# Optimization experiments

Hardware: AMD Instinct MI355X
Metric: run time of the kernel (lower is better)

## Reference

```python
import jax, jax.numpy as jnp
import numpy as np

N0, N1, N2, N3 = 400000, 100000, 20000, 4096
IN_F, HID_F, OUT_F = 256, 256, 128
E0, E1, E2 = 1500000, 200000, 40960


def setup_inputs() -> dict:
    key = jax.random.key(0)
    ks = jax.random.split(key, 16)
    inp = {}
    inp['feat'] = jax.random.normal(ks[0], (N0, IN_F), dtype=jnp.float32)
    inp['e0_src'] = jax.random.randint(ks[1], (E0,), 0, N0)
    inp['e0_dst'] = jax.random.randint(ks[2], (E0,), 0, N1)
    inp['e1_src'] = jax.random.randint(ks[3], (E1,), 0, N1)
    inp['e1_dst'] = jax.random.randint(ks[4], (E1,), 0, N2)
    inp['e2_src'] = jax.random.randint(ks[5], (E2,), 0, N2)
    inp['e2_dst'] = jax.random.randint(ks[6], (E2,), 0, N3)
    # SAGEConv params: fc_self and fc_neigh weights (in,out) + shared bias
    def lin(k, fi, fo):
        s = 1.0 / np.sqrt(fi)
        return jax.random.uniform(k, (fi, fo), jnp.float32, -s, s)
    inp['w_self0'] = lin(ks[7], IN_F, HID_F)
    inp['w_neigh0'] = lin(ks[8], IN_F, HID_F)
    inp['b0'] = jnp.zeros((HID_F,), jnp.float32)
    inp['w_self1'] = lin(ks[9], HID_F, HID_F)
    inp['w_neigh1'] = lin(ks[10], HID_F, HID_F)
    inp['b1'] = jnp.zeros((HID_F,), jnp.float32)
    inp['w_self2'] = lin(ks[11], HID_F, OUT_F)
    inp['w_neigh2'] = lin(ks[12], HID_F, OUT_F)
    inp['b2'] = jnp.zeros((OUT_F,), jnp.float32)
    return inp


def _sage_conv(h, src, dst, n_dst, w_self, w_neigh, b, act):
    # mean aggregation of src-node features onto dst nodes (irregular gather + segment reduce)
    msgs = h[src]                                                  # [E, F]
    s = jax.ops.segment_sum(msgs, dst, num_segments=n_dst)        # [n_dst, F]
    cnt = jax.ops.segment_sum(jnp.ones((src.shape[0], 1), h.dtype), dst, num_segments=n_dst)
    h_neigh = s / jnp.maximum(cnt, 1.0)
    out = h[:n_dst] @ w_self + h_neigh @ w_neigh + b
    return jax.nn.relu(out) if act else out


def reference(feat, e0_src, e0_dst, e1_src, e1_dst, e2_src, e2_dst,
              w_self0, w_neigh0, b0, w_self1, w_neigh1, b1, w_self2, w_neigh2, b2):
    # dropout is identity (eval mode)
    h = _sage_conv(feat, e0_src, e0_dst, N1, w_self0, w_neigh0, b0, act=True)
    h = _sage_conv(h, e1_src, e1_dst, N2, w_self1, w_neigh1, b1, act=True)
    h = _sage_conv(h, e2_src, e2_dst, N3, w_self2, w_neigh2, b2, act=False)
    return h
```

## Files before the change

### kernel.cpp

```cpp
#include <hip/hip_runtime.h>
#include <hip/hip_bf16.h>


static constexpr int kN1 = 100000, kN2 = 20000, kN3 = 4096;
static constexpr int kE0 = 1500000, kE1 = 200000, kE2 = 40960;

using bf8v  = __attribute__((ext_vector_type(8))) short;
using f32x4 = __attribute__((ext_vector_type(4))) float;

__device__ __forceinline__ unsigned short f2bu(float f) {
    __hip_bfloat16 h = __float2bfloat16(f);
    return *reinterpret_cast<unsigned short*>(&h);
}
__device__ __forceinline__ float bu2f_lo(unsigned u) {
    unsigned b = u << 16; return *reinterpret_cast<float*>(&b);
}
__device__ __forceinline__ float bu2f_hi(unsigned u) {
    unsigned b = u & 0xffff0000u; return *reinterpret_cast<float*>(&b);
}

static constexpr int CB  = 50000;
static constexpr int C0B = (kE0 + 255) / 256;
static constexpr int C1B = (kE1 + 255) / 256;
static constexpr int C2B = (kE2 + 255) / 256;
static constexpr int PW0B = 512, PW1B = 512, PW2B = 256;
static constexpr int M4_0 = kN1 / 4, M4_1 = kN2 / 4, M4_2 = kN3 / 4;
static constexpr int B0 = (M4_0 + 255) / 256;
static constexpr int B1 = (M4_1 + 255) / 256;
static constexpr int B2 = (M4_2 + 255) / 256;
static constexpr int ZN4 = (kN1 + kN2 + kN3) / 4;
static constexpr int ZB  = (ZN4 + 255) / 256;

__global__ __launch_bounds__(256) void k_zero(int4* __restrict__ p)
{
    int i = blockIdx.x * 256 + threadIdx.x;
    if (i < ZN4) p[i] = make_int4(0, 0, 0, 0);
}

template <bool BIG>
__global__ __launch_bounds__(256) void k_phase0(
    const float4* __restrict__ feat4, uint4* __restrict__ featbf,
    const int* __restrict__ e0d, const int* __restrict__ e1d,
    const int* __restrict__ e2d,
    int* __restrict__ cnt0, int* __restrict__ cnt1, int* __restrict__ cnt2,
    const float* __restrict__ ws0, const float* __restrict__ wn0,
    const float* __restrict__ ws1, const float* __restrict__ wn1,
    const float* __restrict__ ws2, const float* __restrict__ wn2,
    unsigned short* __restrict__ wt0, unsigned short* __restrict__ wt1,
    unsigned short* __restrict__ wt2)
{
    int b = blockIdx.x;
    const int tid = threadIdx.x;
    if (BIG) {
        if (b < CB) {
            int i = b * 256 + tid;
            float4 a = feat4[2 * i], c = feat4[2 * i + 1];
            uint4 o;
            o.x = (unsigned)f2bu(a.x) | ((unsigned)f2bu(a.y) << 16);
            o.y = (unsigned)f2bu(a.z) | ((unsigned)f2bu(a.w) << 16);
            o.z = (unsigned)f2bu(c.x) | ((unsigned)f2bu(c.y) << 16);
            o.w = (unsigned)f2bu(c.z) | ((unsigned)f2bu(c.w) << 16);
            featbf[i] = o;
            return;
        }
        b -= CB;
    }
    if (b < C0B) {
        int e = b * 256 + tid;
        if (e < kE0) atomicAdd(cnt0 + e0d[e], 1);
        return;
    }
    b -= C0B;
    if (b < C1B) {
        int e = b * 256 + tid;
        if (e < kE1) atomicAdd(cnt1 + e1d[e], 1);
        return;
    }
    b -= C1B;
    if (b < C2B) {
        int e = b * 256 + tid;
        if (e < kE2) atomicAdd(cnt2 + e2d[e], 1);
        return;
    }
    b -= C2B;
    if (b < PW0B) {
        int idx = b * 256 + tid;
        int n = idx >> 9, k = idx & 511;
        wt0[idx] = f2bu(k < 256 ? ws0[k * 256 + n] : wn0[(k - 256) * 256 + n]);
        return;
    }
    b -= PW0B;
    if (b < PW1B) {
        int idx = b * 256 + tid;
        int n = idx >> 9, k = idx & 511;
        wt1[idx] = f2bu(k < 256 ? ws1[k * 256 + n] : wn1[(k - 256) * 256 + n]);
        return;
    }
    b -= PW1B;
    {
        int idx = b * 256 + tid;
        int n = idx >> 9, k = idx & 511;
        wt2[idx] = f2bu(k < 256 ? ws2[k * 128 + n] : wn2[(k - 256) * 128 + n]);
    }
}

__global__ __launch_bounds__(256) void k_bsum_all(
    const int* __restrict__ cnt0, const int* __restrict__ cnt1,
    const int* __restrict__ cnt2, int* __restrict__ bsum)
{
    const int* cnt; int lb, M4, bo;
    int b = blockIdx.x;
    if (b < B0)            { cnt = cnt0; lb = b;            M4 = M4_0; bo = 0; }
    else if (b < B0 + B1)  { cnt = cnt1; lb = b - B0;       M4 = M4_1; bo = B0; }
    else                   { cnt = cnt2; lb = b - B0 - B1;  M4 = M4_2; bo = B0 + B1; }
    __shared__ int wsum[4];
    int idx = lb * 256 + threadIdx.x;
    int ts = 0;
    if (idx < M4) {
        int4 v = reinterpret_cast<const int4*>(cnt)[idx];
        ts = v.x + v.y + v.z + v.w;
    }
#pragma unroll
    for (int off = 32; off > 0; off >>= 1) ts += __shfl_down(ts, off, 64);
    if ((threadIdx.x & 63) == 0) wsum[threadIdx.x >> 6] = ts;
    __syncthreads();
    if (threadIdx.x == 0)
        bsum[bo + lb] = wsum[0] + wsum[1] + wsum[2] + wsum[3];
}

__global__ __launch_bounds__(256) void k_bscan_all(int* __restrict__ bsum)
{
    __shared__ int s[B0 + B1 + B2];
    const int total = B0 + B1 + B2;
    if (threadIdx.x < total) s[threadIdx.x] = bsum[threadIdx.x];
    __syncthreads();
    if (threadIdx.x < 3) {
        int lo = threadIdx.x == 0 ? 0 : (threadIdx.x == 1 ? B0 : B0 + B1);
        int hi = threadIdx.x == 0 ? B0 : (threadIdx.x == 1 ? B0 + B1 : total);
        int run = 0;
        for (int i = lo; i < hi; ++i) { int v = s[i]; s[i] = run; run += v; }
    }
    __syncthreads();
    if (threadIdx.x < total) bsum[threadIdx.x] = s[threadIdx.x];
}

__global__ __launch_bounds__(256) void k_bapply_all(
    const int* __restrict__ cnt0, const int* __restrict__ cnt1,
    const int* __restrict__ cnt2, const int* __restrict__ bsum,
    int* __restrict__ rp0, int* __restrict__ rp1, int* __restrict__ rp2)
{
    const int* cnt; int* rp; int lb, M4, bo;
    int b = blockIdx.x;
    if (b < B0)            { cnt = cnt0; rp = rp0; lb = b;           M4 = M4_0; bo = 0; }
    else if (b < B0 + B1)  { cnt = cnt1; rp = rp1; lb = b - B0;      M4 = M4_1; bo = B0; }
    else                   { cnt = cnt2; rp = rp2; lb = b - B0 - B1; M4 = M4_2; bo = B0 + B1; }
    __shared__ int wsum[4];
    __shared__ int wexcl[4];
    const int lane = threadIdx.x & 63;
    const int wid = threadIdx.x >> 6;
    int idx = lb * 256 + threadIdx.x;
    int4 v = make_int4(0, 0, 0, 0);
    if (idx < M4) v = reinterpret_cast<const int4*>(cnt)[idx];
    int ts = v.x + v.y + v.z + v.w;
    int incl = ts;
#pragma unroll
    for (int off = 1; off < 64; off <<= 1) {
        int t = __shfl_up(incl, off, 64);
        if (lane >= off) incl += t;
    }
    if (lane == 63) wsum[wid] = incl;
    __syncthreads();
    if (threadIdx.x < 4) {
        int e = 0;
        for (int i = 0; i < (int)threadIdx.x; ++i) e += wsum[i];
        wexcl[threadIdx.x] = e;
    }
    __syncthreads();
    if (idx < M4) {
        int base = bsum[bo + lb] + wexcl[wid] + (incl - ts);
        int4 o;
        o.x = base;
        o.y = base + v.x;
        o.z = base + v.x + v.y;
        o.w = base + v.x + v.y + v.z;
        reinterpret_cast<int4*>(rp)[idx] = o;
    }
}

__global__ __launch_bounds__(256) void k_fill_all(
    const int* __restrict__ e0s, const int* __restrict__ e0d,
    const int* __restrict__ e1s, const int* __restrict__ e1d,
    const int* __restrict__ e2s, const int* __restrict__ e2d,
    int* __restrict__ rp0, int* __restrict__ rp1, int* __restrict__ rp2,
    int* __restrict__ csr0, int* __restrict__ csr1, int* __restrict__ csr2)
{
    int b = blockIdx.x;
    const int* src; const int* dst; int* rp; int* csr; int E, lb;
    if (b < C0B)            { src = e0s; dst = e0d; rp = rp0; csr = csr0; E = kE0; lb = b; }
    else if (b < C0B + C1B) { src = e1s; dst = e1d; rp = rp1; csr = csr1; E = kE1; lb = b - C0B; }
    else                    { src = e2s; dst = e2d; rp = rp2; csr = csr2; E = kE2; lb = b - C0B - C1B; }
    int e = lb * 256 + threadIdx.x;
    if (e < E) {
        int pos = atomicAdd(rp + dst[e], 1);
        csr[pos] = src[e];
    }
}

__global__ __launch_bounds__(256) void k_gather_agg_b(
    const unsigned short* __restrict__ h, const int* __restrict__ csr,
    const int* __restrict__ rp_end, const int* __restrict__ cnt,
    unsigned short* __restrict__ agg, int M)
{
    int d = blockIdx.x * 4 + (threadIdx.x >> 6);
    if (d >= M) return;
    const int lane = threadIdx.x & 63;
    const int half = lane >> 5;
    const int l32 = lane & 31;
    int c = cnt[d], end = rp_end[d], start = end - c;
    float a[8] = {0.f, 0.f, 0.f, 0.f, 0.f, 0.f, 0.f, 0.f};
    for (int chunk = start; chunk < end; chunk += 64) {
        int n = end - chunk; if (n > 64) n = 64;
        int mysrc = (lane < n) ? csr[chunk + lane] : 0;
#pragma unroll 4
        for (int e = 0; e < n; e += 2) {
            int ie = e + half;
            int s = __shfl(mysrc, ie, 64);
            if (ie < n) {
                uint4 v = *reinterpret_cast<const uint4*>(
                    h + (size_t)s * 256 + l32 * 8);
                a[0] += bu2f_lo(v.x); a[1] += bu2f_hi(v.x);
                a[2] += bu2f_lo(v.y); a[3] += bu2f_hi(v.y);
                a[4] += bu2f_lo(v.z); a[5] += bu2f_hi(v.z);
                a[6] += bu2f_lo(v.w); a[7] += bu2f_hi(v.w);
            }
        }
    }
#pragma unroll
    for (int j = 0; j < 8; ++j) a[j] += __shfl(a[j], lane ^ 32, 64);
    if (half == 0) {
        float inv = 1.0f / (float)(c > 1 ? c : 1);
        uint4 o;
        o.x = (unsigned)f2bu(a[0] * inv) | ((unsigned)f2bu(a[1] * inv) << 16);
        o.y = (unsigned)f2bu(a[2] * inv) | ((unsigned)f2bu(a[3] * inv) << 16);
        o.z = (unsigned)f2bu(a[4] * inv) | ((unsigned)f2bu(a[5] * inv) << 16);
        o.w = (unsigned)f2bu(a[6] * inv) | ((unsigned)f2bu(a[7] * inv) << 16);
        *reinterpret_cast<uint4*>(agg + (size_t)d * 256 + l32 * 8) = o;
    }
}

__global__ __launch_bounds__(256) void k_gather_agg_f(
    const float* __restrict__ h, const int* __restrict__ csr,
    const int* __restrict__ rp_end, const int* __restrict__ cnt,
    unsigned short* __restrict__ agg, int M)
{
    int d = blockIdx.x * 4 + (threadIdx.x >> 6);
    if (d >= M) return;
    int lane = threadIdx.x & 63;
    int c = cnt[d], end = rp_end[d], start = end - c;
    float a0 = 0.f, a1 = 0.f, a2 = 0.f, a3 = 0.f;
    for (int chunk = start; chunk < end; chunk += 64) {
        int n = end - chunk; if (n > 64) n = 64;
        int mysrc = (lane < n) ? csr[chunk + lane] : 0;
#pragma unroll 4
        for (int e = 0; e < n; ++e) {
            int s = __shfl(mysrc, e, 64);
            float4 v = reinterpret_cast<const float4*>(h + (size_t)s * 256)[lane];
            a0 += v.x; a1 += v.y; a2 += v.z; a3 += v.w;
        }
    }
    float inv = 1.0f / (float)(c > 1 ? c : 1);
    ushort4 o;
    o.x = f2bu(a0 * inv); o.y = f2bu(a1 * inv);
    o.z = f2bu(a2 * inv); o.w = f2bu(a3 * inv);
    *reinterpret_cast<ushort4*>(agg + (size_t)d * 256 + lane * 4) = o;
}

template <int ACT, bool A0F32, bool OUTF32>
__global__ __launch_bounds__(256) void k_mfma_gemm(
    const void* __restrict__ A0v, const unsigned short* __restrict__ A1,
    const unsigned short* __restrict__ WT, const float* __restrict__ bias,
    void* __restrict__ outv, int M, int N)
{
    __shared__ unsigned short sA[128 * 72];
    __shared__ unsigned short sB[128 * 72];
    const int tid = threadIdx.x;
    const int lane = tid & 63;
    const int w = tid >> 6;
    const int wr = w >> 1, wc = w & 1;
    const int row0 = blockIdx.x * 128;
    const int col0 = blockIdx.y * 128;

    f32x4 acc[4][4] = {};

    for (int p = 0; p < 8; ++p) {
        const int kc0 = p * 64;
        if (kc0 < 256) {
            if constexpr (A0F32) {
                const float* src = (const float*)A0v;
#pragma unroll
                for (int ps = 0; ps < 8; ++ps) {
                    int flat = (ps * 256 + tid) * 4;
                    int r = flat >> 6, cc = flat & 63;
                    int row = row0 + r; row = row < M ? row : M - 1;
                    float4 v = *reinterpret_cast<const float4*>(
                        src + (size_t)row * 256 + kc0 + cc);
                    ushort4 b4;
                    b4.x = f2bu(v.x); b4.y = f2bu(v.y);
                    b4.z = f2bu(v.z); b4.w = f2bu(v.w);
                    *reinterpret_cast<ushort4*>(&sA[r * 72 + cc]) = b4;
                }
            } else {
                const unsigned short* src = (const unsigned short*)A0v;
#pragma unroll
                for (int ps = 0; ps < 4; ++ps) {
                    int f8 = ps * 256 + tid;
                    int r = f8 >> 3, c8 = f8 & 7;
                    int row = row0 + r; row = row < M ? row : M - 1;
                    uint4 v = *reinterpret_cast<const uint4*>(
                        src + (size_t)row * 256 + kc0 + c8 * 8);
                    *reinterpret_cast<uint4*>(&sA[r * 72 + c8 * 8]) = v;
                }
            }
        } else {
#pragma unroll
            for (int ps = 0; ps < 4; ++ps) {
                int f8 = ps * 256 + tid;
                int r = f8 >> 3, c8 = f8 & 7;
                int row = row0 + r; row = row < M ? row : M - 1;
                uint4 v = *reinterpret_cast<const uint4*>(
                    A1 + (size_t)row * 256 + (kc0 - 256) + c8 * 8);
                *reinterpret_cast<uint4*>(&sA[r * 72 + c8 * 8]) = v;
            }
        }
#pragma unroll
        for (int ps = 0; ps < 4; ++ps) {
            int f8 = ps * 256 + tid;
            int r = f8 >> 3, c8 = f8 & 7;
            uint4 v = *reinterpret_cast<const uint4*>(
                WT + (size_t)(col0 + r) * 512 + kc0 + c8 * 8);
            *reinterpret_cast<uint4*>(&sB[r * 72 + c8 * 8]) = v;
        }
        __syncthreads();
#pragma unroll
        for (int ks = 0; ks < 64; ks += 32) {
            const int lr = lane & 15;
            const int kk = ks + (lane >> 4) * 8;
            bf8v af[4], bfr[4];
#pragma unroll
            for (int m = 0; m < 4; ++m)
                af[m] = *reinterpret_cast<const bf8v*>(
                    &sA[(wr * 64 + m * 16 + lr) * 72 + kk]);
#pragma unroll
            for (int n = 0; n < 4; ++n)
                bfr[n] = *reinterpret_cast<const bf8v*>(
                    &sB[(wc * 64 + n * 16 + lr) * 72 + kk]);
#pragma unroll
            for (int m = 0; m < 4; ++m)
#pragma unroll
                for (int n = 0; n < 4; ++n)
                    acc[m][n] = __builtin_amdgcn_mfma_f32_16x16x32_bf16(
                        af[m], bfr[n], acc[m][n], 0, 0, 0);
        }
        __syncthreads();
    }

    const int lc = lane & 15;
    const int lr4 = (lane >> 4) * 4;
#pragma unroll
    for (int n = 0; n < 4; ++n) {
        int col = col0 + wc * 64 + n * 16 + lc;
        float bb = bias[col];
#pragma unroll
        for (int m = 0; m < 4; ++m) {
#pragma unroll
            for (int j = 0; j < 4; ++j) {
                int row = row0 + wr * 64 + m * 16 + lr4 + j;
                if (row < M) {
                    float v = acc[m][n][j] + bb;
                    if (ACT) v = fmaxf(v, 0.f);
                    if constexpr (OUTF32)
                        ((float*)outv)[(size_t)row * N + col] = v;
                    else
                        ((unsigned short*)outv)[(size_t)row * N + col] = f2bu(v);
                }
            }
        }
    }
}

extern "C" void kernel_launch(void* const* d_in, const int* in_sizes, int n_in,
                              void* d_out, int out_size, void* d_ws, size_t ws_size,
                              hipStream_t stream) {
    const float* feat = (const float*)d_in[0];
    const int* e0s = (const int*)d_in[1];
    const int* e0d = (const int*)d_in[2];
    const int* e1s = (const int*)d_in[3];
    const int* e1d = (const int*)d_in[4];
    const int* e2s = (const int*)d_in[5];
    const int* e2d = (const int*)d_in[6];
    const float* ws0 = (const float*)d_in[7];
    const float* wn0 = (const float*)d_in[8];
    const float* b0 = (const float*)d_in[9];
    const float* ws1 = (const float*)d_in[10];
    const float* wn1 = (const float*)d_in[11];
    const float* b1 = (const float*)d_in[12];
    const float* ws2 = (const float*)d_in[13];
    const float* wn2 = (const float*)d_in[14];
    const float* b2 = (const float*)d_in[15];
    float* out = (float*)d_out;

    char* base = (char*)d_ws;
    const bool big = ws_size >= 330000000ull;
    unsigned short* featbf = nullptr;
    size_t off = 0;
    if (big) { featbf = (unsigned short*)base; off += 204800000ull; }
    unsigned short* aggb = (unsigned short*)(base + off); off += 51200000ull;
    unsigned short* h1b  = (unsigned short*)(base + off); off += 51200000ull;
    unsigned short* h2b  = (unsigned short*)(base + off); off += 10240000ull;
    unsigned short* wt0  = (unsigned short*)(base + off); off += 262144ull;
    unsigned short* wt1  = (unsigned short*)(base + off); off += 262144ull;
    unsigned short* wt2  = (unsigned short*)(base + off); off += 131072ull;
    int* csr0 = (int*)(base + off); off += 6000000ull;
    int* csr1 = (int*)(base + off); off += 800000ull;
    int* csr2 = (int*)(base + off); off += 163840ull;
    int* cnt0 = (int*)(base + off); off += 400000ull;
    int* cnt1 = (int*)(base + off); off += 80000ull;
    int* cnt2 = (int*)(base + off); off += 16384ull;
    int* rp0  = (int*)(base + off); off += 400000ull;
    int* rp1  = (int*)(base + off); off += 80000ull;
    int* rp2  = (int*)(base + off); off += 16384ull;
    int* bsum = (int*)(base + off); off += 512ull;

    k_zero<<<ZB, 256, 0, stream>>>((int4*)cnt0);

    if (big)
        k_phase0<true><<<CB + C0B + C1B + C2B + PW0B + PW1B + PW2B, 256, 0, stream>>>(
            (const float4*)feat, (uint4*)featbf, e0d, e1d, e2d,
            cnt0, cnt1, cnt2, ws0, wn0, ws1, wn1, ws2, wn2, wt0, wt1, wt2);
    else
        k_phase0<false><<<C0B + C1B + C2B + PW0B + PW1B + PW2B, 256, 0, stream>>>(
            nullptr, nullptr, e0d, e1d, e2d,
            cnt0, cnt1, cnt2, ws0, wn0, ws1, wn1, ws2, wn2, wt0, wt1, wt2);

    k_bsum_all<<<B0 + B1 + B2, 256, 0, stream>>>(cnt0, cnt1, cnt2, bsum);
    k_bscan_all<<<1, 256, 0, stream>>>(bsum);
    k_bapply_all<<<B0 + B1 + B2, 256, 0, stream>>>(
        cnt0, cnt1, cnt2, bsum, rp0, rp1, rp2);
    k_fill_all<<<C0B + C1B + C2B, 256, 0, stream>>>(
        e0s, e0d, e1s, e1d, e2s, e2d, rp0, rp1, rp2, csr0, csr1, csr2);

    if (big) {
        k_gather_agg_b<<<(kN1 + 3) / 4, 256, 0, stream>>>(
            featbf, csr0, rp0, cnt0, aggb, kN1);
        k_mfma_gemm<1, false, false><<<dim3(782, 2), 256, 0, stream>>>(
            featbf, aggb, wt0, b0, h1b, kN1, 256);
    } else {
        k_gather_agg_f<<<(kN1 + 3) / 4, 256, 0, stream>>>(
            feat, csr0, rp0, cnt0, aggb, kN1);
        k_mfma_gemm<1, true, false><<<dim3(782, 2), 256, 0, stream>>>(
            feat, aggb, wt0, b0, h1b, kN1, 256);
    }

    k_gather_agg_b<<<(kN2 + 3) / 4, 256, 0, stream>>>(
        h1b, csr1, rp1, cnt1, aggb, kN2);
    k_mfma_gemm<1, false, false><<<dim3(157, 2), 256, 0, stream>>>(
        h1b, aggb, wt1, b1, h2b, kN2, 256);

    k_gather_agg_b<<<(kN3 + 3) / 4, 256, 0, stream>>>(
        h2b, csr2, rp2, cnt2, aggb, kN3);
    k_mfma_gemm<0, false, true><<<dim3(32, 1), 256, 0, stream>>>(
        h2b, aggb, wt2, b2, out, kN3, 128);
}
```

Before: 565.1 us.

## Fuse CSR-build front-end kernels into one persistent kernel with grid barriers

Replaces the phase0, block-sum, block-scan, scan-apply and fill kernels with a single persistent kernel of 1024 blocks. The blocks loop over virtual block indices and separate the phases with atomic-counter grid barriers. The zeroed region is widened so the barrier counters are cleared each call. This removes four kernel launches and their gaps. The costs are fewer resident blocks for the large streaming conversion phase and spin-wait barriers, which deadlock if all 1024 blocks are not co-resident.

```diff
diff --git a/kernel.cpp b/kernel.cpp
--- a/kernel.cpp
+++ b/kernel.cpp
@@ -28,8 +28,10 @@
 static constexpr int B0 = (M4_0 + 255) / 256;
 static constexpr int B1 = (M4_1 + 255) / 256;
 static constexpr int B2 = (M4_2 + 255) / 256;
-static constexpr int ZN4 = (kN1 + kN2 + kN3) / 4;
+static constexpr int BSCAN = B0 + B1 + B2;
+static constexpr int ZN4 = 496448 / 16;
 static constexpr int ZB  = (ZN4 + 255) / 256;
+static constexpr int NB = 1024;
 
 __global__ __launch_bounds__(256) void k_zero(int4* __restrict__ p)
 {
@@ -37,172 +39,174 @@
     if (i < ZN4) p[i] = make_int4(0, 0, 0, 0);
 }
 
+__device__ __forceinline__ void gbar(int* ctr)
+{
+    __syncthreads();
+    if (threadIdx.x == 0) {
+        __threadfence();
+        atomicAdd(ctr, 1);
+        while (atomicAdd(ctr, 0) < NB) __builtin_amdgcn_s_sleep(8);
+        __threadfence();
+    }
+    __syncthreads();
+}
+
 template <bool BIG>
-__global__ __launch_bounds__(256) void k_phase0(
+__global__ __launch_bounds__(256, 4) void k_megafront(
     const float4* __restrict__ feat4, uint4* __restrict__ featbf,
-    const int* __restrict__ e0d, const int* __restrict__ e1d,
-    const int* __restrict__ e2d,
+    const int* __restrict__ e0s, const int* __restrict__ e0d,
+    const int* __restrict__ e1s, const int* __restrict__ e1d,
+    const int* __restrict__ e2s, const int* __restrict__ e2d,
     int* __restrict__ cnt0, int* __restrict__ cnt1, int* __restrict__ cnt2,
     const float* __restrict__ ws0, const float* __restrict__ wn0,
     const float* __restrict__ ws1, const float* __restrict__ wn1,
     const float* __restrict__ ws2, const float* __restrict__ wn2,
     unsigned short* __restrict__ wt0, unsigned short* __restrict__ wt1,
-    unsigned short* __restrict__ wt2)
-{
-    int b = blockIdx.x;
+    unsigned short* __restrict__ wt2,
+    int* __restrict__ bsum,
+    int* __restrict__ rp0, int* __restrict__ rp1, int* __restrict__ rp2,
+    int* __restrict__ csr0, int* __restrict__ csr1, int* __restrict__ csr2,
+    int* __restrict__ gctr)
+{
+    __shared__ int smem[128];
+    __shared__ int sreg[128];
     const int tid = threadIdx.x;
-    if (BIG) {
-        if (b < CB) {
-            int i = b * 256 + tid;
-            float4 a = feat4[2 * i], c = feat4[2 * i + 1];
-            uint4 o;
-            o.x = (unsigned)f2bu(a.x) | ((unsigned)f2bu(a.y) << 16);
-            o.y = (unsigned)f2bu(a.z) | ((unsigned)f2bu(a.w) << 16);
-            o.z = (unsigned)f2bu(c.x) | ((unsigned)f2bu(c.y) << 16);
-            o.w = (unsigned)f2bu(c.z) | ((unsigned)f2bu(c.w) << 16);
-            featbf[i] = o;
-            return;
-        }
-        b -= CB;
-    }
-    if (b < C0B) {
-        int e = b * 256 + tid;
-        if (e < kE0) atomicAdd(cnt0 + e0d[e], 1);
-        return;
-    }
-    b -= C0B;
-    if (b < C1B) {
-        int e = b * 256 + tid;
-        if (e < kE1) atomicAdd(cnt1 + e1d[e], 1);
-        return;
-    }
-    b -= C1B;
-    if (b < C2B) {
-        int e = b * 256 + tid;
-        if (e < kE2) atomicAdd(cnt2 + e2d[e], 1);
-        return;
-    }
-    b -= C2B;
-    if (b < PW0B) {
-        int idx = b * 256 + tid;
-        int n = idx >> 9, k = idx & 511;
-        wt0[idx] = f2bu(k < 256 ? ws0[k * 256 + n] : wn0[(k - 256) * 256 + n]);
-        return;
-    }
-    b -= PW0B;
-    if (b < PW1B) {
-        int idx = b * 256 + tid;
-        int n = idx >> 9, k = idx & 511;
-        wt1[idx] = f2bu(k < 256 ? ws1[k * 256 + n] : wn1[(k - 256) * 256 + n]);
-        return;
-    }
-    b -= PW1B;
-    {
-        int idx = b * 256 + tid;
-        int n = idx >> 9, k = idx & 511;
-        wt2[idx] = f2bu(k < 256 ? ws2[k * 128 + n] : wn2[(k - 256) * 128 + n]);
-    }
-}
-
-__global__ __launch_bounds__(256) void k_bsum_all(
-    const int* __restrict__ cnt0, const int* __restrict__ cnt1,
-    const int* __restrict__ cnt2, int* __restrict__ bsum)
-{
-    const int* cnt; int lb, M4, bo;
-    int b = blockIdx.x;
-    if (b < B0)            { cnt = cnt0; lb = b;            M4 = M4_0; bo = 0; }
-    else if (b < B0 + B1)  { cnt = cnt1; lb = b - B0;       M4 = M4_1; bo = B0; }
-    else                   { cnt = cnt2; lb = b - B0 - B1;  M4 = M4_2; bo = B0 + B1; }
-    __shared__ int wsum[4];
-    int idx = lb * 256 + threadIdx.x;
-    int ts = 0;
-    if (idx < M4) {
-        int4 v = reinterpret_cast<const int4*>(cnt)[idx];
-        ts = v.x + v.y + v.z + v.w;
-    }
-#pragma unroll
-    for (int off = 32; off > 0; off >>= 1) ts += __shfl_down(ts, off, 64);
-    if ((threadIdx.x & 63) == 0) wsum[threadIdx.x >> 6] = ts;
-    __syncthreads();
-    if (threadIdx.x == 0)
-        bsum[bo + lb] = wsum[0] + wsum[1] + wsum[2] + wsum[3];
-}
-
-__global__ __launch_bounds__(256) void k_bscan_all(int* __restrict__ bsum)
-{
-    __shared__ int s[B0 + B1 + B2];
-    const int total = B0 + B1 + B2;
-    if (threadIdx.x < total) s[threadIdx.x] = bsum[threadIdx.x];
-    __syncthreads();
-    if (threadIdx.x < 3) {
-        int lo = threadIdx.x == 0 ? 0 : (threadIdx.x == 1 ? B0 : B0 + B1);
-        int hi = threadIdx.x == 0 ? B0 : (threadIdx.x == 1 ? B0 + B1 : total);
-        int run = 0;
-        for (int i = lo; i < hi; ++i) { int v = s[i]; s[i] = run; run += v; }
-    }
-    __syncthreads();
-    if (threadIdx.x < total) bsum[threadIdx.x] = s[threadIdx.x];
-}
-
-__global__ __launch_bounds__(256) void k_bapply_all(
-    const int* __restrict__ cnt0, const int* __restrict__ cnt1,
-    const int* __restrict__ cnt2, const int* __restrict__ bsum,
-    int* __restrict__ rp0, int* __restrict__ rp1, int* __restrict__ rp2)
-{
-    const int* cnt; int* rp; int lb, M4, bo;
-    int b = blockIdx.x;
-    if (b < B0)            { cnt = cnt0; rp = rp0; lb = b;           M4 = M4_0; bo = 0; }
-    else if (b < B0 + B1)  { cnt = cnt1; rp = rp1; lb = b - B0;      M4 = M4_1; bo = B0; }
-    else                   { cnt = cnt2; rp = rp2; lb = b - B0 - B1; M4 = M4_2; bo = B0 + B1; }
-    __shared__ int wsum[4];
-    __shared__ int wexcl[4];
-    const int lane = threadIdx.x & 63;
-    const int wid = threadIdx.x >> 6;
-    int idx = lb * 256 + threadIdx.x;
-    int4 v = make_int4(0, 0, 0, 0);
-    if (idx < M4) v = reinterpret_cast<const int4*>(cnt)[idx];
-    int ts = v.x + v.y + v.z + v.w;
-    int incl = ts;
-#pragma unroll
-    for (int off = 1; off < 64; off <<= 1) {
-        int t = __shfl_up(incl, off, 64);
-        if (lane >= off) incl += t;
-    }
-    if (lane == 63) wsum[wid] = incl;
-    __syncthreads();
-    if (threadIdx.x < 4) {
-        int e = 0;
-        for (int i = 0; i < (int)threadIdx.x; ++i) e += wsum[i];
-        wexcl[threadIdx.x] = e;
-    }
-    __syncthreads();
-    if (idx < M4) {
-        int base = bsum[bo + lb] + wexcl[wid] + (incl - ts);
-        int4 o;
-        o.x = base;
-        o.y = base + v.x;
-        o.z = base + v.x + v.y;
-        o.w = base + v.x + v.y + v.z;
-        reinterpret_cast<int4*>(rp)[idx] = o;
-    }
-}
-
-__global__ __launch_bounds__(256) void k_fill_all(
-    const int* __restrict__ e0s, const int* __restrict__ e0d,
-    const int* __restrict__ e1s, const int* __restrict__ e1d,
-    const int* __restrict__ e2s, const int* __restrict__ e2d,
-    int* __restrict__ rp0, int* __restrict__ rp1, int* __restrict__ rp2,
-    int* __restrict__ csr0, int* __restrict__ csr1, int* __restrict__ csr2)
-{
-    int b = blockIdx.x;
-    const int* src; const int* dst; int* rp; int* csr; int E, lb;
-    if (b < C0B)            { src = e0s; dst = e0d; rp = rp0; csr = csr0; E = kE0; lb = b; }
-    else if (b < C0B + C1B) { src = e1s; dst = e1d; rp = rp1; csr = csr1; E = kE1; lb = b - C0B; }
-    else                    { src = e2s; dst = e2d; rp = rp2; csr = csr2; E = kE2; lb = b - C0B - C1B; }
-    int e = lb * 256 + threadIdx.x;
-    if (e < E) {
-        int pos = atomicAdd(rp + dst[e], 1);
-        csr[pos] = src[e];
+
+    const int P0 = (BIG ? CB : 0) + C0B + C1B + C2B + PW0B + PW1B + PW2B;
+    for (int vb = blockIdx.x; vb < P0; vb += NB) {
+        int b = vb;
+        bool done = false;
+        if (BIG) {
+            if (b < CB) {
+                int i = b * 256 + tid;
+                float4 a = feat4[2 * i], c = feat4[2 * i + 1];
+                uint4 o;
+                o.x = (unsigned)f2bu(a.x) | ((unsigned)f2bu(a.y) << 16);
+                o.y = (unsigned)f2bu(a.z) | ((unsigned)f2bu(a.w) << 16);
+                o.z = (unsigned)f2bu(c.x) | ((unsigned)f2bu(c.y) << 16);
+                o.w = (unsigned)f2bu(c.z) | ((unsigned)f2bu(c.w) << 16);
+                featbf[i] = o;
+                done = true;
+            } else b -= CB;
+        }
+        if (!done && b < C0B) {
+            int e = b * 256 + tid;
+            if (e < kE0) atomicAdd(cnt0 + e0d[e], 1);
+            done = true;
+        } else if (!done) b -= C0B;
+        if (!done && b < C1B) {
+            int e = b * 256 + tid;
+            if (e < kE1) atomicAdd(cnt1 + e1d[e], 1);
+            done = true;
+        } else if (!done) b -= C1B;
+        if (!done && b < C2B) {
+            int e = b * 256 + tid;
+            if (e < kE2) atomicAdd(cnt2 + e2d[e], 1);
+            done = true;
+        } else if (!done) b -= C2B;
+        if (!done && b < PW0B) {
+            int idx = b * 256 + tid;
+            int n = idx >> 9, k = idx & 511;
+            wt0[idx] = f2bu(k < 256 ? ws0[k * 256 + n] : wn0[(k - 256) * 256 + n]);
+            done = true;
+        } else if (!done) b -= PW0B;
+        if (!done && b < PW1B) {
+            int idx = b * 256 + tid;
+            int n = idx >> 9, k = idx & 511;
+            wt1[idx] = f2bu(k < 256 ? ws1[k * 256 + n] : wn1[(k - 256) * 256 + n]);
+            done = true;
+        } else if (!done) b -= PW1B;
+        if (!done) {
+            int idx = b * 256 + tid;
+            int n = idx >> 9, k = idx & 511;
+            wt2[idx] = f2bu(k < 256 ? ws2[k * 128 + n] : wn2[(k - 256) * 128 + n]);
+        }
+    }
+    gbar(gctr + 0);
+
+    for (int vb = blockIdx.x; vb < BSCAN; vb += NB) {
+        const int* cnt; int lb, M4, bo;
+        if (vb < B0)           { cnt = cnt0; lb = vb;           M4 = M4_0; bo = 0; }
+        else if (vb < B0 + B1) { cnt = cnt1; lb = vb - B0;      M4 = M4_1; bo = B0; }
+        else                   { cnt = cnt2; lb = vb - B0 - B1; M4 = M4_2; bo = B0 + B1; }
+        int idx = lb * 256 + tid;
+        int ts = 0;
+        if (idx < M4) {
+            int4 v = reinterpret_cast<const int4*>(cnt)[idx];
+            ts = v.x + v.y + v.z + v.w;
+        }
+#pragma unroll
+        for (int off = 32; off > 0; off >>= 1) ts += __shfl_down(ts, off, 64);
+        if ((tid & 63) == 0) smem[tid >> 6] = ts;
+        __syncthreads();
+        if (tid == 0) bsum[bo + lb] = smem[0] + smem[1] + smem[2] + smem[3];
+        __syncthreads();
+    }
+    gbar(gctr + 1);
+
+    if (blockIdx.x == 0) {
+        if (tid < BSCAN) smem[tid] = bsum[tid];
+        __syncthreads();
+        if (tid < 3) {
+            int lo = tid == 0 ? 0 : (tid == 1 ? B0 : B0 + B1);
+            int hi = tid == 0 ? B0 : (tid == 1 ? B0 + B1 : BSCAN);
+            int run = 0;
+            for (int i = lo; i < hi; ++i) { int v = smem[i]; smem[i] = run; run += v; }
+        }
+        __syncthreads();
+        if (tid < BSCAN) bsum[tid] = smem[tid];
+    }
+    gbar(gctr + 2);
+
+    for (int vb = blockIdx.x; vb < BSCAN; vb += NB) {
+        const int* cnt; int* rp; int lb, M4, bo;
+        if (vb < B0)           { cnt = cnt0; rp = rp0; lb = vb;           M4 = M4_0; bo = 0; }
+        else if (vb < B0 + B1) { cnt = cnt1; rp = rp1; lb = vb - B0;      M4 = M4_1; bo = B0; }
+        else                   { cnt = cnt2; rp = rp2; lb = vb - B0 - B1; M4 = M4_2; bo = B0 + B1; }
+        const int lane = tid & 63;
+        const int wid = tid >> 6;
+        int idx = lb * 256 + tid;
+        int4 v = make_int4(0, 0, 0, 0);
+        if (idx < M4) v = reinterpret_cast<const int4*>(cnt)[idx];
+        int ts = v.x + v.y + v.z + v.w;
+        int incl = ts;
+#pragma unroll
+        for (int off = 1; off < 64; off <<= 1) {
+            int t = __shfl_up(incl, off, 64);
+            if (lane >= off) incl += t;
+        }
+        if (lane == 63) smem[wid] = incl;
+        __syncthreads();
+        if (tid < 4) {
+            int e = 0;
+            for (int i = 0; i < tid; ++i) e += smem[i];
+            sreg[tid] = e;
+        }
+        __syncthreads();
+        if (idx < M4) {
+            int base = bsum[bo + lb] + sreg[wid] + (incl - ts);
+            int4 o;
+            o.x = base;
+            o.y = base + v.x;
+            o.z = base + v.x + v.y;
+            o.w = base + v.x + v.y + v.z;
+            reinterpret_cast<int4*>(rp)[idx] = o;
+        }
+        __syncthreads();
+    }
+    gbar(gctr + 3);
+
+    const int PF = C0B + C1B + C2B;
+    for (int vb = blockIdx.x; vb < PF; vb += NB) {
+        const int* src; const int* dst; int* rp; int* csr; int E, lb;
+        if (vb < C0B)           { src = e0s; dst = e0d; rp = rp0; csr = csr0; E = kE0; lb = vb; }
+        else if (vb < C0B + C1B){ src = e1s; dst = e1d; rp = rp1; csr = csr1; E = kE1; lb = vb - C0B; }
+        else                    { src = e2s; dst = e2d; rp = rp2; csr = csr2; E = kE2; lb = vb - C0B - C1B; }
+        int e = lb * 256 + tid;
+        if (e < E) {
+            int pos = atomicAdd(rp + dst[e], 1);
+            csr[pos] = src[e];
+        }
     }
 }
 
@@ -426,6 +430,7 @@
     int* cnt0 = (int*)(base + off); off += 400000ull;
     int* cnt1 = (int*)(base + off); off += 80000ull;
     int* cnt2 = (int*)(base + off); off += 16384ull;
+    int* gctr = (int*)(base + off); off += 64ull;
     int* rp0  = (int*)(base + off); off += 400000ull;
     int* rp1  = (int*)(base + off); off += 80000ull;
     int* rp2  = (int*)(base + off); off += 16384ull;
@@ -434,20 +439,19 @@
     k_zero<<<ZB, 256, 0, stream>>>((int4*)cnt0);
 
     if (big)
-        k_phase0<true><<<CB + C0B + C1B + C2B + PW0B + PW1B + PW2B, 256, 0, stream>>>(
-            (const float4*)feat, (uint4*)featbf, e0d, e1d, e2d,
-            cnt0, cnt1, cnt2, ws0, wn0, ws1, wn1, ws2, wn2, wt0, wt1, wt2);
+        k_megafront<true><<<NB, 256, 0, stream>>>(
+            (const float4*)feat, (uint4*)featbf,
+            e0s, e0d, e1s, e1d, e2s, e2d,
+            cnt0, cnt1, cnt2,
+            ws0, wn0, ws1, wn1, ws2, wn2, wt0, wt1, wt2,
+            bsum, rp0, rp1, rp2, csr0, csr1, csr2, gctr);
     else
-        k_phase0<false><<<C0B + C1B + C2B + PW0B + PW1B + PW2B, 256, 0, stream>>>(
-            nullptr, nullptr, e0d, e1d, e2d,
-            cnt0, cnt1, cnt2, ws0, wn0, ws1, wn1, ws2, wn2, wt0, wt1, wt2);
-
-    k_bsum_all<<<B0 + B1 + B2, 256, 0, stream>>>(cnt0, cnt1, cnt2, bsum);
-    k_bscan_all<<<1, 256, 0, stream>>>(bsum);
-    k_bapply_all<<<B0 + B1 + B2, 256, 0, stream>>>(
-        cnt0, cnt1, cnt2, bsum, rp0, rp1, rp2);
-    k_fill_all<<<C0B + C1B + C2B, 256, 0, stream>>>(
-        e0s, e0d, e1s, e1d, e2s, e2d, rp0, rp1, rp2, csr0, csr1, csr2);
+        k_megafront<false><<<NB, 256, 0, stream>>>(
+            nullptr, nullptr,
+            e0s, e0d, e1s, e1d, e2s, e2d,
+            cnt0, cnt1, cnt2,
+            ws0, wn0, ws1, wn1, ws2, wn2, wt0, wt1, wt2,
+            bsum, rp0, rp1, rp2, csr0, csr1, csr2, gctr);
 
     if (big) {
         k_gather_agg_b<<<(kN1 + 3) / 4, 256, 0, stream>>>(
```

After: 937.7 us. 65.9% more time.
